# Kernel tuning notes

Hardware: AMD Instinct MI355X
Metric: run time of the kernel (lower is better)

Reference implementation:

```python
import jax, jax.numpy as jnp
import numpy as np

NUM_LAYERS = 2


def setup_inputs() -> dict:
    key = jax.random.key(0)
    ks = jax.random.split(key, 8)
    B, S, D, H, O, L = 32, 2048, 512, 512, 512, NUM_LAYERS
    stdv = 1.0 / np.sqrt(H)
    u = lambda k, shape: jax.random.uniform(k, shape, jnp.float32, -stdv, stdv)
    return {
        "x": jax.random.normal(ks[0], (B, S, D), jnp.float32),
        "hidden": jnp.zeros((L, B, H), jnp.float32),
        "w_ih": u(ks[1], (L, H, D)),
        "w_hh": u(ks[2], (L, H, H)),
        "b_ih": u(ks[3], (L, H)),
        "b_hh": u(ks[4], (L, H)),
        "w_out": u(ks[5], (O, H)),
        "b_out": u(ks[6], (O,)),
    }


def reference(x, hidden, w_ih, w_hh, b_ih, b_hh, w_out, b_out):
    # x: [B, S, D]; hidden: [L, B, H]
    L = w_ih.shape[0]

    def step(h, x_t):  # h: [L, B, H], x_t: [B, D]
        new_hs = []
        inp = x_t
        for l in range(L):
            h_new = jnp.tanh(inp @ w_ih[l].T + b_ih[l] + h[l] @ w_hh[l].T + b_hh[l])
            new_hs.append(h_new)
            inp = h_new
        return jnp.stack(new_hs), inp  # carry, output of top layer

    xs = jnp.swapaxes(x, 0, 1)  # [S, B, D]
    _, outs = jax.lax.scan(step, hidden, xs)  # outs: [S, B, H]
    rnn_out = jnp.swapaxes(outs, 0, 1)  # [B, S, H]
    return rnn_out @ w_out.T + b_out  # [B, S, O]
```

## Files before the change

kernel.cpp:

```cpp
#include <hip/hip_runtime.h>


typedef short v8s __attribute__((ext_vector_type(8)));
typedef int   v4i __attribute__((ext_vector_type(4)));
typedef float v4f __attribute__((ext_vector_type(4)));

#define B_  32
#define S_  2048
#define DH  512
#define SLOT32 16384
#define EPOCH4(q) ((unsigned)(((q) >> 2) & 7))

#define BIAS_OFF  0
#define H0_OFF    8192
#define H1_OFF    (H0_OFF + 4 * 65536)
#define WOUT_OFF  (H1_OFF + 4 * 65536)
#define WIH0_OFF  (WOUT_OFF + 524288)

#define PART_BYTES (8 * 3 * 4 * 64 * 16)

static __device__ __forceinline__ unsigned short f2bf(float f) {
  unsigned int u = __builtin_bit_cast(unsigned int, f);
  u += 0x7fffu + ((u >> 16) & 1u);
  return (unsigned short)(u >> 16);
}
static __device__ __forceinline__ float bf2f(unsigned short h) {
  return __builtin_bit_cast(float, ((unsigned int)h) << 16);
}
static __device__ __forceinline__ unsigned packh(float f, unsigned ep) {
  unsigned short hv = f2bf(f);
  unsigned short lv = f2bf(f - bf2f(hv));
  return ((unsigned)hv << 16) | ((unsigned)lv & 0xFFF8u) | ep;
}
static __device__ __forceinline__ v8s pack8(float4 f0, float4 f1) {
  v8s r;
  r[0] = (short)f2bf(f0.x); r[1] = (short)f2bf(f0.y);
  r[2] = (short)f2bf(f0.z); r[3] = (short)f2bf(f0.w);
  r[4] = (short)f2bf(f1.x); r[5] = (short)f2bf(f1.y);
  r[6] = (short)f2bf(f1.z); r[7] = (short)f2bf(f1.w);
  return r;
}
static __device__ __forceinline__ float fast_tanh(float v) {
  float c = fminf(15.f, fmaxf(-15.f, v));
  float e = __expf(2.f * c);
  return (e - 1.f) * __builtin_amdgcn_rcpf(e + 1.f);
}

static __device__ __forceinline__ v4i ld16v(const unsigned* p) {
  v4i r;
  asm volatile("global_load_dwordx4 %0, %1, off sc1"
               : "=v"(r) : "v"(p) : "memory");
  return r;
}
static __device__ __forceinline__ float ld4(const void* p) {
  float r;
  asm volatile("global_load_dword %0, %1, off"
               : "=v"(r) : "v"(p) : "memory");
  return r;
}
static __device__ __forceinline__ void atom_swap(void* p, unsigned v) {
  asm volatile("global_atomic_swap %0, %1, off"
               :: "v"(p), "v"(v) : "memory");
}
#define WAITN0() do { asm volatile("s_waitcnt vmcnt(0)" ::: "memory"); \
    __builtin_amdgcn_sched_barrier(0); } while (0)

static __device__ __forceinline__ void poll_frag(const unsigned* b, unsigned ep,
                                                 bool* bad, v4i* o0, v4i* o1,
                                                 v4i* o2, v4i* o3) {
  v4i a0, a1, a2, a3;
  int t = 0;
  for (;;) {
    a0 = ld16v(b); a1 = ld16v(b + 4); a2 = ld16v(b + 32); a3 = ld16v(b + 36);
    WAITN0();
    if (*bad) break;
    unsigned d = 0;
    #pragma unroll
    for (int j = 0; j < 4; ++j)
      d |= ((unsigned)a0[j] ^ ep) | ((unsigned)a1[j] ^ ep)
         | ((unsigned)a2[j] ^ ep) | ((unsigned)a3[j] ^ ep);
    if (__all((d & 7u) == 0u)) break;
    if (++t > (1 << 15)) { *bad = true; break; }
  }
  *o0 = a0; *o1 = a1; *o2 = a2; *o3 = a3;
}
static __device__ __forceinline__ void unp(v4i a, v4i b, v8s* hi, v8s* lo) {
  v8s h, l;
  #pragma unroll
  for (int j = 0; j < 4; ++j) {
    unsigned ua = (unsigned)a[j], ub = (unsigned)b[j];
    h[j]     = (short)(ua >> 16);   l[j]     = (short)(ua & 0xFFF8u);
    h[4 + j] = (short)(ub >> 16);   l[4 + j] = (short)(ub & 0xFFF8u);
  }
  *hi = h; *lo = l;
}

__global__ void rnn_init(const float* __restrict__ hidden,
                         const float* __restrict__ b_ih,
                         const float* __restrict__ b_hh,
                         const float* __restrict__ w_out,
                         const float* __restrict__ w_ih,
                         float* __restrict__ bias,
                         unsigned* __restrict__ h0ring,
                         unsigned* __restrict__ h1ring,
                         unsigned short* __restrict__ woutbf,
                         unsigned short* __restrict__ wih0bf) {
  int i = blockIdx.x * blockDim.x + threadIdx.x;
  int nth = gridDim.x * blockDim.x;
  for (int t = i; t < 1024; t += nth) bias[t] = b_ih[t] + b_hh[t];
  for (int t = i; t < 2 * B_ * DH; t += nth) {
    int l = t >> 14;
    int off = t & 16383;
    unsigned* ring = l ? h1ring : h0ring;
    atom_swap(ring + 3 * SLOT32 + off, packh(hidden[t], 7u));
  }
  for (int t = i; t < 512 * 512; t += nth) {
    woutbf[t] = f2bf(w_out[t]);
    wih0bf[t] = f2bf(w_ih[t]);
  }
}

__global__ __launch_bounds__(512) void proj64(
    const float* __restrict__ src,
    float* __restrict__ dst,
    const unsigned short* __restrict__ wb,
    const float* __restrict__ bias) {
  __shared__ unsigned short lds[64 * 512];
  const int tid = threadIdx.x;
  const int wid = tid >> 6;
  const int lane = tid & 63;
  const size_t row0 = (size_t)blockIdx.x * 64;

  #pragma unroll
  for (int it = 0; it < 8; ++it) {
    int c = it * 512 + tid;
    int row = c >> 6;
    int col8 = c & 63;
    const float4* s4 = (const float4*)(src + (row0 + row) * DH + col8 * 8);
    float4 f0 = s4[0], f1 = s4[1];
    v8s t = pack8(f0, f1);
    int byteoff = row * 1024 + ((col8 * 16) ^ ((row & 7) << 4));
    *(v8s*)((char*)lds + byteoff) = t;
  }
  __syncthreads();

  const int l15 = lane & 15;
  const int kq = (lane >> 4) * 8;

  for (int nt = wid; nt < 32; nt += 8) {
    v4f acc[4];
    #pragma unroll
    for (int mt = 0; mt < 4; ++mt) acc[mt] = (v4f){0.f, 0.f, 0.f, 0.f};
    const unsigned short* wr = wb + (size_t)(nt * 16 + l15) * 512;
    #pragma unroll
    for (int ks = 0; ks < 16; ++ks) {
      int kk = ks * 32 + kq;
      v8s bfrag = *(const v8s*)(wr + kk);
      #pragma unroll
      for (int mt = 0; mt < 4; ++mt) {
        int row = mt * 16 + l15;
        int byteoff = row * 1024 + ((kk * 2) ^ ((row & 7) << 4));
        v8s afrag = *(const v8s*)((char*)lds + byteoff);
        acc[mt] = __builtin_amdgcn_mfma_f32_16x16x32_bf16(afrag, bfrag, acc[mt], 0, 0, 0);
      }
    }
    float bo = bias[nt * 16 + l15];
    #pragma unroll
    for (int mt = 0; mt < 4; ++mt)
      #pragma unroll
      for (int r = 0; r < 4; ++r) {
        int row = mt * 16 + (lane >> 4) * 4 + r;
        int col = nt * 16 + l15;
        dst[(row0 + row) * DH + col] = acc[mt][r] + bo;
      }
  }
}

__global__ __launch_bounds__(512) void rnn_fused(
    const float* __restrict__ z0,
    const float* __restrict__ w_ih,
    const float* __restrict__ w_hh,
    const float* __restrict__ bias,
    unsigned* __restrict__ h0ring,
    unsigned* __restrict__ h1ring,
    float* __restrict__ dout) {
  extern __shared__ char smem[];
  v4f* part = (v4f*)smem;

  const int wg = blockIdx.x;
  const int mh = wg >> 3;
  const int fs = wg & 7;

  const int tid = threadIdx.x;
  const int wid = tid >> 6;
  const int lane = tid & 63;
  const int l15 = lane & 15;
  const int kq = (lane >> 4) * 8;
  const int q4 = (lane >> 4) * 4;

  v8s wfrag[3][4][2];
  {
    const float* wsrcs[3] = { w_hh, w_ih + 512 * 512, w_hh + 512 * 512 };
    #pragma unroll
    for (int g = 0; g < 3; ++g)
      #pragma unroll
      for (int n = 0; n < 4; ++n)
        #pragma unroll
        for (int ks = 0; ks < 2; ++ks) {
          const float* srow = wsrcs[g] +
              (size_t)(fs * 64 + n * 16 + l15) * 512 + wid * 64 + ks * 32 + kq;
          wfrag[g][n][ks] = pack8(*(const float4*)srow, *(const float4*)(srow + 4));
        }
  }
  const int nf = wid & 3;
  const float bias1v = bias[512 + fs * 64 + nf * 16 + l15];
  const size_t abase = (size_t)(mh * 16 + l15) * 512 + wid * 64 + kq;
  const int featf = fs * 64 + nf * 16 + l15;

  bool bad = false;

  for (int p = 0; p <= S_; ++p) {
    float zp[4];
    if (wid < 4) {
      const int pz = (p < S_) ? p : (S_ - 1);
      #pragma unroll
      for (int r = 0; r < 4; ++r)
        zp[r] = ld4(z0 + ((size_t)(mh * 16 + q4 + r) * S_ + pz) * DH + featf);
    }

    const unsigned ep0 = (p == 0) ? 7u : EPOCH4(p - 1);
    const unsigned* h0b = h0ring + (size_t)((p + 3) & 3) * SLOT32 + abase;
    v4i A0, A1, A2, A3;
    poll_frag(h0b, ep0, &bad, &A0, &A1, &A2, &A3);
    v8s h0h0, h0l0, h0h1, h0l1;
    unp(A0, A1, &h0h0, &h0l0);
    unp(A2, A3, &h0h1, &h0l1);

    v4f acc0[4], acc1[4], acc2[4];
    #pragma unroll
    for (int n = 0; n < 4; ++n) {
      acc0[n] = (v4f){0.f, 0.f, 0.f, 0.f};
      acc1[n] = (v4f){0.f, 0.f, 0.f, 0.f};
      acc2[n] = (v4f){0.f, 0.f, 0.f, 0.f};
    }
    #pragma unroll
    for (int n = 0; n < 4; ++n) {
      acc0[n] = __builtin_amdgcn_mfma_f32_16x16x32_bf16(h0h0, wfrag[0][n][0], acc0[n], 0, 0, 0);
      acc0[n] = __builtin_amdgcn_mfma_f32_16x16x32_bf16(h0l0, wfrag[0][n][0], acc0[n], 0, 0, 0);
      acc0[n] = __builtin_amdgcn_mfma_f32_16x16x32_bf16(h0h1, wfrag[0][n][1], acc0[n], 0, 0, 0);
      acc0[n] = __builtin_amdgcn_mfma_f32_16x16x32_bf16(h0l1, wfrag[0][n][1], acc0[n], 0, 0, 0);
      acc1[n] = __builtin_amdgcn_mfma_f32_16x16x32_bf16(h0h0, wfrag[1][n][0], acc1[n], 0, 0, 0);
      acc1[n] = __builtin_amdgcn_mfma_f32_16x16x32_bf16(h0l0, wfrag[1][n][0], acc1[n], 0, 0, 0);
      acc1[n] = __builtin_amdgcn_mfma_f32_16x16x32_bf16(h0h1, wfrag[1][n][1], acc1[n], 0, 0, 0);
      acc1[n] = __builtin_amdgcn_mfma_f32_16x16x32_bf16(h0l1, wfrag[1][n][1], acc1[n], 0, 0, 0);
    }

    if (p >= 1) {
      const unsigned ep1 = (p == 1) ? 7u : EPOCH4(p - 2);
      const unsigned* h1b = h1ring + (size_t)((p + 2) & 3) * SLOT32 + abase;
      v4i B0, B1, B2, B3;
      poll_frag(h1b, ep1, &bad, &B0, &B1, &B2, &B3);
      v8s h1h0, h1l0, h1h1, h1l1;
      unp(B0, B1, &h1h0, &h1l0);
      unp(B2, B3, &h1h1, &h1l1);
      #pragma unroll
      for (int n = 0; n < 4; ++n) {
        acc2[n] = __builtin_amdgcn_mfma_f32_16x16x32_bf16(h1h0, wfrag[2][n][0], acc2[n], 0, 0, 0);
        acc2[n] = __builtin_amdgcn_mfma_f32_16x16x32_bf16(h1l0, wfrag[2][n][0], acc2[n], 0, 0, 0);
        acc2[n] = __builtin_amdgcn_mfma_f32_16x16x32_bf16(h1h1, wfrag[2][n][1], acc2[n], 0, 0, 0);
        acc2[n] = __builtin_amdgcn_mfma_f32_16x16x32_bf16(h1l1, wfrag[2][n][1], acc2[n], 0, 0, 0);
      }
    }

    #pragma unroll
    for (int n = 0; n < 4; ++n) {
      part[((wid * 3 + 0) * 4 + n) * 64 + lane] = acc0[n];
      part[((wid * 3 + 1) * 4 + n) * 64 + lane] = acc1[n];
      part[((wid * 3 + 2) * 4 + n) * 64 + lane] = acc2[n];
    }
    __syncthreads();

    if (wid < 4) {
      v4f s0 = {0.f,0.f,0.f,0.f}, s1 = {0.f,0.f,0.f,0.f}, s2 = {0.f,0.f,0.f,0.f};
      #pragma unroll
      for (int w = 0; w < 8; ++w) {
        s0 += part[((w * 3 + 0) * 4 + nf) * 64 + lane];
        s1 += part[((w * 3 + 1) * 4 + nf) * 64 + lane];
        s2 += part[((w * 3 + 2) * 4 + nf) * 64 + lane];
      }
      float h0v[4], h1v[4];
      #pragma unroll
      for (int r = 0; r < 4; ++r) {
        h0v[r] = fast_tanh(zp[r] + s0[r]);
        h1v[r] = fast_tanh(s1[r] + s2[r] + bias1v);
      }
      if (p < S_) {
        const unsigned ep = EPOCH4(p);
        unsigned* dst = h0ring + (size_t)(p & 3) * SLOT32;
        #pragma unroll
        for (int r = 0; r < 4; ++r)
          atom_swap(dst + (size_t)(mh * 16 + q4 + r) * 512 + featf,
                    packh(h0v[r], ep));
      }
      if (p >= 1) {
        const unsigned ep = EPOCH4(p - 1);
        unsigned* dst = h1ring + (size_t)((p - 1) & 3) * SLOT32;
        #pragma unroll
        for (int r = 0; r < 4; ++r) {
          atom_swap(dst + (size_t)(mh * 16 + q4 + r) * 512 + featf,
                    packh(h1v[r], ep));
          dout[((size_t)(mh * 16 + q4 + r) * S_ + (p - 1)) * DH + featf] = h1v[r];
        }
      }
    }
    __syncthreads();
  }
}

extern "C" void kernel_launch(void* const* d_in, const int* in_sizes, int n_in,
                              void* d_out, int out_size, void* d_ws, size_t ws_size,
                              hipStream_t stream) {
  const float* x      = (const float*)d_in[0];
  const float* hidden = (const float*)d_in[1];
  const float* w_ih   = (const float*)d_in[2];
  const float* w_hh   = (const float*)d_in[3];
  const float* b_ih   = (const float*)d_in[4];
  const float* b_hh   = (const float*)d_in[5];
  const float* w_out  = (const float*)d_in[6];
  const float* b_out  = (const float*)d_in[7];
  float* out = (float*)d_out;

  char* wsb = (char*)d_ws;
  float* bias            = (float*)(wsb + BIAS_OFF);
  unsigned* h0ring       = (unsigned*)(wsb + H0_OFF);
  unsigned* h1ring       = (unsigned*)(wsb + H1_OFF);
  unsigned short* woutbf = (unsigned short*)(wsb + WOUT_OFF);
  unsigned short* wih0bf = (unsigned short*)(wsb + WIH0_OFF);

  rnn_init<<<256, 256, 0, stream>>>(hidden, b_ih, b_hh, w_out, w_ih,
                                    bias, h0ring, h1ring, woutbf, wih0bf);
  proj64<<<(B_ * S_) / 64, 512, 0, stream>>>(x, out, wih0bf, bias);
  rnn_fused<<<16, 512, PART_BYTES, stream>>>(out, w_ih, w_hh, bias,
                                             h0ring, h1ring, out);
  proj64<<<(B_ * S_) / 64, 512, 0, stream>>>(out, out, woutbf, b_out);
}
```

Baseline: 7.245 ms.

## Pipeline hidden-state polling with double-buffered loads and split MFMA halves

Replaces the blocking poll of the full layer-0 hidden fragment with a double-buffered poll on the first half, keeping two loads in flight. Once the first half is ready, it issues the second-half and layer-1 loads and runs the first-half MFMAs while they are in flight. The later fragments are checked for the expected epoch and are only re-polled if they are stale. The aim is to cut the per-step latency of spinning on cross-workgroup hidden-state handoff, at the cost of more complex wait logic and extra in-flight loads.

```diff
diff --git a/kernel.cpp b/kernel.cpp
--- a/kernel.cpp
+++ b/kernel.cpp
@@ -63,6 +63,8 @@
                :: "v"(p), "v"(v) : "memory");
 }
 #define WAITN0() do { asm volatile("s_waitcnt vmcnt(0)" ::: "memory"); \
+    __builtin_amdgcn_sched_barrier(0); } while (0)
+#define WAIT2() do { asm volatile("s_waitcnt vmcnt(2)" ::: "memory"); \
     __builtin_amdgcn_sched_barrier(0); } while (0)
 
 static __device__ __forceinline__ void poll_frag(const unsigned* b, unsigned ep,
@@ -220,6 +222,41 @@
   bool bad = false;
 
   for (int p = 0; p <= S_; ++p) {
+    const unsigned ep0 = (p == 0) ? 7u : EPOCH4(p - 1);
+    const unsigned ep1 = (p == 1) ? 7u : EPOCH4(p - 2);
+    const unsigned* h0b = h0ring + (size_t)((p + 3) & 3) * SLOT32 + abase;
+    const unsigned* h1b = h1ring + (size_t)((p + 2) & 3) * SLOT32 + abase;
+
+    v4i Pa0 = ld16v(h0b); v4i Pa1 = ld16v(h0b + 4);
+    v4i Pb0 = ld16v(h0b); v4i Pb1 = ld16v(h0b + 4);
+    v4i F0, F1;
+    {
+      int t = 0;
+      for (;;) {
+        WAIT2();
+        unsigned d = 0;
+        #pragma unroll
+        for (int j = 0; j < 4; ++j)
+          d |= ((unsigned)Pa0[j] ^ ep0) | ((unsigned)Pa1[j] ^ ep0);
+        if (__all((d & 7u) == 0u) || bad) { F0 = Pa0; F1 = Pa1; break; }
+        Pa0 = ld16v(h0b); Pa1 = ld16v(h0b + 4);
+        WAIT2();
+        d = 0;
+        #pragma unroll
+        for (int j = 0; j < 4; ++j)
+          d |= ((unsigned)Pb0[j] ^ ep0) | ((unsigned)Pb1[j] ^ ep0);
+        if (__all((d & 7u) == 0u)) { F0 = Pb0; F1 = Pb1; break; }
+        Pb0 = ld16v(h0b); Pb1 = ld16v(h0b + 4);
+        if (++t > (1 << 15)) { bad = true; F0 = Pb0; F1 = Pb1; break; }
+      }
+    }
+
+    v4i A2 = ld16v(h0b + 32), A3 = ld16v(h0b + 36);
+    v4i B0, B1, B2, B3;
+    if (p >= 1) {
+      B0 = ld16v(h1b); B1 = ld16v(h1b + 4);
+      B2 = ld16v(h1b + 32); B3 = ld16v(h1b + 36);
+    }
     float zp[4];
     if (wid < 4) {
       const int pz = (p < S_) ? p : (S_ - 1);
@@ -228,13 +265,8 @@
         zp[r] = ld4(z0 + ((size_t)(mh * 16 + q4 + r) * S_ + pz) * DH + featf);
     }
 
-    const unsigned ep0 = (p == 0) ? 7u : EPOCH4(p - 1);
-    const unsigned* h0b = h0ring + (size_t)((p + 3) & 3) * SLOT32 + abase;
-    v4i A0, A1, A2, A3;
-    poll_frag(h0b, ep0, &bad, &A0, &A1, &A2, &A3);
-    v8s h0h0, h0l0, h0h1, h0l1;
-    unp(A0, A1, &h0h0, &h0l0);
-    unp(A2, A3, &h0h1, &h0l1);
+    v8s h0h0, h0l0;
+    unp(F0, F1, &h0h0, &h0l0);
 
     v4f acc0[4], acc1[4], acc2[4];
     #pragma unroll
@@ -247,19 +279,51 @@
     for (int n = 0; n < 4; ++n) {
       acc0[n] = __builtin_amdgcn_mfma_f32_16x16x32_bf16(h0h0, wfrag[0][n][0], acc0[n], 0, 0, 0);
       acc0[n] = __builtin_amdgcn_mfma_f32_16x16x32_bf16(h0l0, wfrag[0][n][0], acc0[n], 0, 0, 0);
+      acc1[n] = __builtin_amdgcn_mfma_f32_16x16x32_bf16(h0h0, wfrag[1][n][0], acc1[n], 0, 0, 0);
+      acc1[n] = __builtin_amdgcn_mfma_f32_16x16x32_bf16(h0l0, wfrag[1][n][0], acc1[n], 0, 0, 0);
+    }
+
+    WAITN0();
+    asm volatile("" :: "v"(Pa0), "v"(Pa1), "v"(Pb0), "v"(Pb1));
+
+    {
+      unsigned d = 0;
+      #pragma unroll
+      for (int j = 0; j < 4; ++j)
+        d |= ((unsigned)A2[j] ^ ep0) | ((unsigned)A3[j] ^ ep0);
+      if (!__all((d & 7u) == 0u)) {
+        int t = 0;
+        for (;;) {
+          A2 = ld16v(h0b + 32); A3 = ld16v(h0b + 36);
+          WAITN0();
+          if (bad) break;
+          d = 0;
+          #pragma unroll
+          for (int j = 0; j < 4; ++j)
+            d |= ((unsigned)A2[j] ^ ep0) | ((unsigned)A3[j] ^ ep0);
+          if (__all((d & 7u) == 0u)) break;
+          if (++t > (1 << 15)) { bad = true; break; }
+        }
+      }
+    }
+    v8s h0h1, h0l1;
+    unp(A2, A3, &h0h1, &h0l1);
+    #pragma unroll
+    for (int n = 0; n < 4; ++n) {
       acc0[n] = __builtin_amdgcn_mfma_f32_16x16x32_bf16(h0h1, wfrag[0][n][1], acc0[n], 0, 0, 0);
       acc0[n] = __builtin_amdgcn_mfma_f32_16x16x32_bf16(h0l1, wfrag[0][n][1], acc0[n], 0, 0, 0);
-      acc1[n] = __builtin_amdgcn_mfma_f32_16x16x32_bf16(h0h0, wfrag[1][n][0], acc1[n], 0, 0, 0);
-      acc1[n] = __builtin_amdgcn_mfma_f32_16x16x32_bf16(h0l0, wfrag[1][n][0], acc1[n], 0, 0, 0);
       acc1[n] = __builtin_amdgcn_mfma_f32_16x16x32_bf16(h0h1, wfrag[1][n][1], acc1[n], 0, 0, 0);
       acc1[n] = __builtin_amdgcn_mfma_f32_16x16x32_bf16(h0l1, wfrag[1][n][1], acc1[n], 0, 0, 0);
     }
 
     if (p >= 1) {
-      const unsigned ep1 = (p == 1) ? 7u : EPOCH4(p - 2);
-      const unsigned* h1b = h1ring + (size_t)((p + 2) & 3) * SLOT32 + abase;
-      v4i B0, B1, B2, B3;
-      poll_frag(h1b, ep1, &bad, &B0, &B1, &B2, &B3);
+      unsigned d = 0;
+      #pragma unroll
+      for (int j = 0; j < 4; ++j)
+        d |= ((unsigned)B0[j] ^ ep1) | ((unsigned)B1[j] ^ ep1)
+           | ((unsigned)B2[j] ^ ep1) | ((unsigned)B3[j] ^ ep1);
+      if (!__all((d & 7u) == 0u))
+        poll_frag(h1b, ep1, &bad, &B0, &B1, &B2, &B3);
       v8s h1h0, h1l0, h1h1, h1l1;
       unp(B0, B1, &h1h0, &h1l0);
       unp(B2, B3, &h1h1, &h1l1);
```

Measured after the change: 8.806 ms. 21.5% more time.
